# Kernel tuning notes

Measured on AMD Instinct MI355X. Metric: run time of the kernel, lower is better.

The kernel has to match this reference:

```python
import jax, jax.numpy as jnp
import numpy as np

B, C, H, W = 8, 384, 32, 32
HEADS = 12


def _relative_position_index(h, w):
    coords_h = np.arange(h)
    coords_w = np.arange(w)
    coords = np.stack(np.meshgrid(coords_h, coords_w, indexing='ij'))  # [2,h,w]
    flat = coords.reshape(2, -1)  # [2, N]
    rel = flat[:, :, None] - flat[:, None, :]  # [2, N, N]
    rel = rel.transpose(1, 2, 0)  # [N, N, 2]
    rel[:, :, 0] += h - 1
    rel[:, :, 1] += w - 1
    rel[:, :, 0] *= 2 * w - 1
    return rel.sum(-1).astype(np.int32)  # [N, N]


def setup_inputs() -> dict:
    key = jax.random.key(0)
    ks = jax.random.split(key, 6)
    std = 0.02
    x = jax.random.normal(ks[0], (B, C, H, W), dtype=jnp.float32)
    q_w = jax.random.normal(ks[1], (C, C), dtype=jnp.float32) * std
    q_b = jnp.zeros((C,), dtype=jnp.float32)
    kv_w = jax.random.normal(ks[2], (2 * C, C), dtype=jnp.float32) * std
    kv_b = jnp.zeros((2 * C,), dtype=jnp.float32)
    proj_w = jax.random.normal(ks[3], (C, C), dtype=jnp.float32) * std
    proj_b = jnp.zeros((C,), dtype=jnp.float32)
    n_table = (2 * H - 1) * (2 * W - 1)
    rpb_table = jax.random.normal(ks[4], (n_table, HEADS), dtype=jnp.float32) * std
    rel_index = jnp.asarray(_relative_position_index(H, W))  # [N, N] int32
    return {"x": x, "q_w": q_w, "q_b": q_b, "kv_w": kv_w, "kv_b": kv_b,
            "proj_w": proj_w, "proj_b": proj_b, "rpb_table": rpb_table,
            "rel_index": rel_index}


def reference(x, q_w, q_b, kv_w, kv_b, proj_w, proj_b, rpb_table, rel_index):
    b, c, h, w = x.shape
    n = h * w
    heads = rpb_table.shape[-1]
    hd = c // heads
    scale = hd ** (-0.5)

    xf = x.reshape(b, c, n)  # 1x1 conv == per-pixel matmul
    q = jnp.einsum('dc,bcn->bdn', q_w, xf) + q_b[:, None]
    q = q.reshape(b, heads, hd, n).transpose(0, 1, 3, 2)  # [b,h,n,hd]
    kv = jnp.einsum('dc,bcn->bdn', kv_w, xf) + kv_b[:, None]
    kv = kv.reshape(b, 2, heads, hd, n)
    k = kv[:, 0].transpose(0, 1, 3, 2)  # [b,h,n,hd]
    v = kv[:, 1].transpose(0, 1, 3, 2)

    attn = jnp.einsum('bhnd,bhmd->bhnm', q, k) * scale  # [b,h,n,n]
    bias = rpb_table[rel_index.reshape(-1)].reshape(n, n, heads)
    bias = bias.transpose(2, 0, 1)  # [h,n,n]
    attn = jax.nn.softmax(attn + bias[None], axis=-1)

    out = jnp.einsum('bhnm,bhmd->bhnd', attn, v)
    out = out.transpose(0, 1, 3, 2).reshape(b, c, h, w)
    out = jnp.einsum('dc,bchw->bdhw', proj_w, out) + proj_b[None, :, None, None]
    return out
```

## Files before the change

kernel.cpp:

```cpp
#include <hip/hip_runtime.h>
#include <hip/hip_bf16.h>

#define B_  8
#define C_  384
#define N_  1024
#define NH_ 12
#define HD_ 32
#define D3_ 1152

typedef __bf16 bf16x8 __attribute__((ext_vector_type(8)));
typedef float  f32x4  __attribute__((ext_vector_type(4)));

typedef const __attribute__((address_space(1))) unsigned int guint;
typedef __attribute__((address_space(3))) unsigned int luint;

__device__ __forceinline__ float b2f(ushort u) {
    return __uint_as_float(((unsigned int)u) << 16);
}
__device__ __forceinline__ ushort f2b(float f) {
    unsigned int i = __float_as_uint(f);
    unsigned int r = i + 0x7fffu + ((i >> 16) & 1u);
    return (ushort)(r >> 16);
}

#if __has_builtin(__builtin_amdgcn_exp2f)
#define EXP2 __builtin_amdgcn_exp2f
#else
#define EXP2 exp2f
#endif

__device__ __forceinline__ void gl2lds16(const void* g, void* l) {
    __builtin_amdgcn_global_load_lds((guint*)g, (luint*)l, 16, 0, 0);
}

__global__ __launch_bounds__(256) void setup(
    const float* __restrict__ x, const float* __restrict__ q_w,
    const float* __restrict__ kv_w, const float* __restrict__ proj_w,
    const float* __restrict__ q_b, const float* __restrict__ kv_b,
    const float* __restrict__ tab,
    ushort* __restrict__ xT, ushort* __restrict__ biasL,
    ushort* __restrict__ Wall, ushort* __restrict__ PW,
    float* __restrict__ ballf)
{
    __shared__ ushort T[64 * 72];
    const int bx = blockIdx.x, tid = threadIdx.x;

    if (bx < 3072) {
        const float C2 = 1.4426950408889634f;
        int gid = bx * 256 + tid;
        int lane = gid & 63;
        int mc = (gid >> 6) & 15;
        int qs = (gid >> 10) & 63;
        int h  = gid >> 16;
        int quad = lane >> 4, l16 = lane & 15;
        int q = qs * 16 + l16;
        int qy = q >> 5, qx = q & 31;
        union { uint4 u[2]; ushort us[16]; } o;
        #pragma unroll
        for (int t = 0; t < 4; ++t) {
            #pragma unroll
            for (int r = 0; r < 4; ++r) {
                int m = mc * 64 + t * 16 + quad * 4 + r;
                int my = m >> 5, mx = m & 31;
                int dy = qy - my + 31, dx = qx - mx + 31;
                float v = tab[(size_t)(dy * 63 + dx) * NH_ + h] * C2;
                o.us[t * 4 + r] = f2b(v);
            }
        }
        ushort* dst = biasL + (size_t)gid * 16;
        *(uint4*)dst = o.u[0];
        *(uint4*)(dst + 8) = o.u[1];
    } else if (bx < 3840) {
        int t = bx - 3072;
        int nx = t & 15, cy = (t >> 4) % 6, b = t / 96;
        int n0 = nx * 64, c0 = cy * 64;
        {
            int i = tid >> 2;
            int ns = (tid & 3) * 16;
            const float* src = x + ((size_t)b * C_ + c0 + i) * N_ + n0 + ns;
            #pragma unroll
            for (int k4 = 0; k4 < 4; ++k4) {
                float4 f = *(const float4*)(src + k4 * 4);
                T[(ns + k4 * 4 + 0) * 72 + i] = f2b(f.x);
                T[(ns + k4 * 4 + 1) * 72 + i] = f2b(f.y);
                T[(ns + k4 * 4 + 2) * 72 + i] = f2b(f.z);
                T[(ns + k4 * 4 + 3) * 72 + i] = f2b(f.w);
            }
        }
        __syncthreads();
        {
            int j = tid >> 2;
            int cs = (tid & 3) * 16;
            ushort* dst = xT + ((size_t)b * N_ + n0 + j) * C_ + c0 + cs;
            *(uint4*)dst       = *(const uint4*)&T[j * 72 + cs];
            *(uint4*)(dst + 8) = *(const uint4*)&T[j * 72 + cs + 8];
        }
    } else {
        const int NW4 = 110592, NP4 = 36864, NB4 = 288;
        int t = (bx - 3840) * 256 + tid;
        if (t < NW4) {
            int e = t * 4;
            float4 f = (e < 147456) ? *(const float4*)(q_w + e)
                                    : *(const float4*)(kv_w + e - 147456);
            union { uint2 u; ushort s[4]; } o;
            o.s[0] = f2b(f.x); o.s[1] = f2b(f.y); o.s[2] = f2b(f.z); o.s[3] = f2b(f.w);
            *(uint2*)(Wall + e) = o.u;
        } else if (t < NW4 + NP4) {
            int e = (t - NW4) * 4;
            float4 f = *(const float4*)(proj_w + e);
            union { uint2 u; ushort s[4]; } o;
            o.s[0] = f2b(f.x); o.s[1] = f2b(f.y); o.s[2] = f2b(f.z); o.s[3] = f2b(f.w);
            *(uint2*)(PW + e) = o.u;
        } else if (t < NW4 + NP4 + NB4) {
            int e = (t - NW4 - NP4) * 4;
            float4 f = (e < 384) ? *(const float4*)(q_b + e)
                                 : *(const float4*)(kv_b + e - 384);
            *(float4*)(ballf + e) = f;
        }
    }
}

__global__ __launch_bounds__(256) void qkv_gemm3(
    const ushort* __restrict__ xT, const ushort* __restrict__ Wall,
    const float* __restrict__ ballf, ushort* __restrict__ Qt,
    ushort* __restrict__ Kt, ushort* __restrict__ Vtmp)
{
    const int b = blockIdx.z, n0 = blockIdx.x * 128, d0 = blockIdx.y * 128;
    __shared__ ushort As[128 * 32];
    __shared__ ushort Bs[128 * 32];
    const int tid = threadIdx.x;
    const int lane = tid & 63, wave = tid >> 6;
    const int quad = lane >> 4, l16 = lane & 15;
    const int wn = (wave & 1) * 64, wd = (wave >> 1) * 64;

    f32x4 acc[4][4] = {};
    const ushort* xb = xT + ((size_t)b * N_ + n0) * C_;
    const ushort* wb = Wall + (size_t)d0 * C_;
    const int rowA = wave * 16 + (lane >> 2);
    const int fstage = ((lane >> 2) ^ (lane >> 4)) & 3;
    const int coff = ((lane & 3) ^ fstage) * 8;
    const int fread = ((l16 & 3) ^ ((l16 >> 2) & 3));

    for (int c0 = 0; c0 < C_; c0 += 32) {
        #pragma unroll
        for (int k = 0; k < 2; ++k) {
            gl2lds16(xb + (size_t)(k * 64 + rowA) * C_ + c0 + coff,
                     &As[(size_t)(k * 256 + wave * 64) * 8]);
            gl2lds16(wb + (size_t)(k * 64 + rowA) * C_ + c0 + coff,
                     &Bs[(size_t)(k * 256 + wave * 64) * 8]);
        }
        __syncthreads();
        bf16x8 af[4], bfr[4];
        #pragma unroll
        for (int i = 0; i < 4; ++i)
            af[i] = *(const bf16x8*)&As[(wn + i * 16 + l16) * 32 + (quad ^ fread) * 8];
        #pragma unroll
        for (int j = 0; j < 4; ++j)
            bfr[j] = *(const bf16x8*)&Bs[(wd + j * 16 + l16) * 32 + (quad ^ fread) * 8];
        #pragma unroll
        for (int i = 0; i < 4; ++i)
            #pragma unroll
            for (int j = 0; j < 4; ++j)
                acc[i][j] = __builtin_amdgcn_mfma_f32_16x16x32_bf16(af[i], bfr[j], acc[i][j], 0, 0, 0);
        __syncthreads();
    }

    ushort* dst; int reg0;
    if (d0 < 384)      { dst = Qt;   reg0 = 0; }
    else if (d0 < 768) { dst = Kt;   reg0 = 384; }
    else               { dst = Vtmp; reg0 = 768; }
    const int hb = (d0 - reg0) >> 5;
    #pragma unroll
    for (int j = 0; j < 4; ++j) {
        int dloc = wd + j * 16 + l16;
        int h = hb + (dloc >> 5), dc = dloc & 31;
        float bv = ballf[d0 + dloc];
        size_t base = ((size_t)(b * NH_ + h) * N_) * 32 + dc;
        #pragma unroll
        for (int i = 0; i < 4; ++i) {
            int nbase = n0 + wn + i * 16 + quad * 4;
            #pragma unroll
            for (int r = 0; r < 4; ++r)
                dst[base + (size_t)(nbase + r) * 32] = f2b(acc[i][j][r] + bv);
        }
    }
}

__global__ __launch_bounds__(256) void vtrans(
    const ushort* __restrict__ Vtmp, ushort* __restrict__ Vtc)
{
    const int mc = blockIdx.x, bh = blockIdx.y;
    __shared__ ushort T[32 * 80];
    const int tid = threadIdx.x;
    {
        int row = tid >> 2;
        int dcs = (tid & 3) * 8;
        union { uint4 u; ushort s[8]; } a;
        a.u = *(const uint4*)(Vtmp + ((size_t)bh * N_ + mc * 64 + row) * 32 + dcs);
        #pragma unroll
        for (int k = 0; k < 8; ++k) T[(dcs + k) * 80 + row] = a.s[k];
    }
    __syncthreads();
    {
        int kc = tid >> 7, dc = (tid >> 2) & 31, mm8 = (tid & 3) * 8;
        *(uint4*)(Vtc + ((size_t)(bh * 16 + mc) * 2 + kc) * 1024 + dc * 32 + mm8) =
            *(const uint4*)&T[dc * 80 + kc * 32 + mm8];
    }
}

__global__ __launch_bounds__(256) void attn3(
    const ushort* __restrict__ Qt, const ushort* __restrict__ Kt,
    const ushort* __restrict__ Vtc, const ushort* __restrict__ biasL,
    ushort* __restrict__ O)
{
    const int bid = blockIdx.x;
    const int nx = bid & 7;
    const int h  = (bid >> 3) % NH_;
    const int b  = bid / 96;
    __shared__ ushort Pa[8192];

    const int tid = threadIdx.x;
    const int lane = tid & 63, wave = tid >> 6;
    const int quad = lane >> 4, l16 = lane & 15;
    const int bh = b * NH_ + h;
    const int qs0 = nx * 8 + wave * 2;

    const ushort* Kbh = Kt + (size_t)bh * N_ * 32;
    const ushort* Vbh = Vtc + (size_t)bh * 16 * 2048;

    bf16x8 qf[2];
    #pragma unroll
    for (int st = 0; st < 2; ++st)
        qf[st] = *(const bf16x8*)(Qt + ((size_t)bh * N_ + (qs0 + st) * 16 + l16) * 32 + quad * 8);

    const ushort* bp[2];
    #pragma unroll
    for (int st = 0; st < 2; ++st)
        bp[st] = biasL + ((size_t)(h * 64 + qs0 + st) * 16 * 64 + lane) * 16;

    f32x4 oacc[2][2] = {};
    float rs[2] = {0.f, 0.f};

    ushort* PwBase = &Pa[wave * 2048];
    const int pswz = l16 & 0xE;
    const float C1 = 0.17677669529663687f * 1.4426950408889634f;
    const f32x4 zero = {0.f, 0.f, 0.f, 0.f};

    for (int mc = 0; mc < 16; ++mc) {
        const ushort* kp = Kbh + mc * 64 * 32;
        bf16x8 k0 = *(const bf16x8*)(kp + (0 * 16 + l16) * 32 + quad * 8);
        bf16x8 k1 = *(const bf16x8*)(kp + (1 * 16 + l16) * 32 + quad * 8);
        bf16x8 k2 = *(const bf16x8*)(kp + (2 * 16 + l16) * 32 + quad * 8);
        bf16x8 k3 = *(const bf16x8*)(kp + (3 * 16 + l16) * 32 + quad * 8);
        const ushort* vp = Vbh + mc * 2048;
        bf16x8 va[2][2];
        #pragma unroll
        for (int kc = 0; kc < 2; ++kc)
            #pragma unroll
            for (int dt = 0; dt < 2; ++dt)
                va[kc][dt] = *(const bf16x8*)(vp + kc * 1024 + (dt * 16 + l16) * 32 + quad * 8);
        union { uint4 u[2]; ushort us[16]; } bw[2];
        #pragma unroll
        for (int st = 0; st < 2; ++st) {
            bw[st].u[0] = *(const uint4*)(bp[st] + mc * 1024);
            bw[st].u[1] = *(const uint4*)(bp[st] + mc * 1024 + 8);
        }

        #pragma unroll
        for (int st = 0; st < 2; ++st) {
            f32x4 s0 = __builtin_amdgcn_mfma_f32_16x16x32_bf16(k0, qf[st], zero, 0, 0, 0);
            f32x4 s1 = __builtin_amdgcn_mfma_f32_16x16x32_bf16(k1, qf[st], zero, 0, 0, 0);
            f32x4 s2 = __builtin_amdgcn_mfma_f32_16x16x32_bf16(k2, qf[st], zero, 0, 0, 0);
            f32x4 s3 = __builtin_amdgcn_mfma_f32_16x16x32_bf16(k3, qf[st], zero, 0, 0, 0);

            ushort* Pw = PwBase + st * 1024;
            f32x4 sv[4] = {s0, s1, s2, s3};
            #pragma unroll
            for (int t = 0; t < 4; ++t) {
                float p0 = EXP2(sv[t][0] * C1 + b2f(bw[st].us[t * 4 + 0]));
                float p1 = EXP2(sv[t][1] * C1 + b2f(bw[st].us[t * 4 + 1]));
                float p2 = EXP2(sv[t][2] * C1 + b2f(bw[st].us[t * 4 + 2]));
                float p3 = EXP2(sv[t][3] * C1 + b2f(bw[st].us[t * 4 + 3]));
                rs[st] += (p0 + p1) + (p2 + p3);
                uint2 w;
                w.x = (unsigned)f2b(p0) | ((unsigned)f2b(p1) << 16);
                w.y = (unsigned)f2b(p2) | ((unsigned)f2b(p3) << 16);
                *(uint2*)(Pw + l16 * 64 + (((t * 4 + quad) ^ pswz) * 4)) = w;
            }
            #pragma unroll
            for (int kc = 0; kc < 2; ++kc) {
                bf16x8 pb = *(const bf16x8*)(Pw + l16 * 64 + (((kc * 8 + quad * 2) ^ pswz) * 4));
                oacc[st][0] = __builtin_amdgcn_mfma_f32_16x16x32_bf16(va[kc][0], pb, oacc[st][0], 0, 0, 0);
                oacc[st][1] = __builtin_amdgcn_mfma_f32_16x16x32_bf16(va[kc][1], pb, oacc[st][1], 0, 0, 0);
            }
        }
    }

    #pragma unroll
    for (int st = 0; st < 2; ++st) {
        float s = rs[st];
        s += __shfl_xor(s, 16, 64);
        s += __shfl_xor(s, 32, 64);
        rs[st] = 1.0f / s;
    }

    #pragma unroll
    for (int st = 0; st < 2; ++st) {
        int q = (qs0 + st) * 16 + l16;
        ushort* ob = O + ((size_t)(b * N_ + q)) * C_ + h * HD_;
        #pragma unroll
        for (int dt = 0; dt < 2; ++dt) {
            float v0 = oacc[st][dt][0] * rs[st];
            float v1 = oacc[st][dt][1] * rs[st];
            float v2 = oacc[st][dt][2] * rs[st];
            float v3 = oacc[st][dt][3] * rs[st];
            uint2 w;
            w.x = (unsigned)f2b(v0) | ((unsigned)f2b(v1) << 16);
            w.y = (unsigned)f2b(v2) | ((unsigned)f2b(v3) << 16);
            *(uint2*)(ob + dt * 16 + quad * 4) = w;
        }
    }
}

__global__ __launch_bounds__(256) void proj_gemm3(
    const ushort* __restrict__ O, const ushort* __restrict__ PW,
    const float* __restrict__ pb, float* __restrict__ out)
{
    const int b = blockIdx.z, n0 = blockIdx.x * 128, d0 = blockIdx.y * 128;
    __shared__ ushort As[128 * 32];
    __shared__ ushort Bs[128 * 32];
    const int tid = threadIdx.x;
    const int lane = tid & 63, wave = tid >> 6;
    const int quad = lane >> 4, l16 = lane & 15;
    const int wa = (wave & 1) * 64, wb = (wave >> 1) * 64;

    f32x4 acc[4][4] = {};
    const ushort* ab = PW + (size_t)d0 * C_;
    const ushort* bbp = O + ((size_t)b * N_ + n0) * C_;
    const int rowA = wave * 16 + (lane >> 2);
    const int fstage = ((lane >> 2) ^ (lane >> 4)) & 3;
    const int coff = ((lane & 3) ^ fstage) * 8;
    const int fread = ((l16 & 3) ^ ((l16 >> 2) & 3));

    for (int c0 = 0; c0 < C_; c0 += 32) {
        #pragma unroll
        for (int k = 0; k < 2; ++k) {
            gl2lds16(ab + (size_t)(k * 64 + rowA) * C_ + c0 + coff,
                     &As[(size_t)(k * 256 + wave * 64) * 8]);
            gl2lds16(bbp + (size_t)(k * 64 + rowA) * C_ + c0 + coff,
                     &Bs[(size_t)(k * 256 + wave * 64) * 8]);
        }
        __syncthreads();
        bf16x8 af[4], bfr[4];
        #pragma unroll
        for (int i = 0; i < 4; ++i)
            af[i] = *(const bf16x8*)&As[(wa + i * 16 + l16) * 32 + (quad ^ fread) * 8];
        #pragma unroll
        for (int j = 0; j < 4; ++j)
            bfr[j] = *(const bf16x8*)&Bs[(wb + j * 16 + l16) * 32 + (quad ^ fread) * 8];
        #pragma unroll
        for (int i = 0; i < 4; ++i)
            #pragma unroll
            for (int j = 0; j < 4; ++j)
                acc[i][j] = __builtin_amdgcn_mfma_f32_16x16x32_bf16(af[i], bfr[j], acc[i][j], 0, 0, 0);
        __syncthreads();
    }

    #pragma unroll
    for (int i = 0; i < 4; ++i) {
        #pragma unroll
        for (int r = 0; r < 4; ++r) {
            int d = d0 + wa + i * 16 + quad * 4 + r;
            float bv = pb[d];
            float* op = out + ((size_t)b * C_ + d) * N_ + n0 + wb;
            #pragma unroll
            for (int j = 0; j < 4; ++j)
                op[j * 16 + l16] = acc[i][j][r] + bv;
        }
    }
}

extern "C" void kernel_launch(void* const* d_in, const int* in_sizes, int n_in,
                              void* d_out, int out_size, void* d_ws, size_t ws_size,
                              hipStream_t stream)
{
    const float* x      = (const float*)d_in[0];
    const float* q_w    = (const float*)d_in[1];
    const float* q_b    = (const float*)d_in[2];
    const float* kv_w   = (const float*)d_in[3];
    const float* kv_b   = (const float*)d_in[4];
    const float* proj_w = (const float*)d_in[5];
    const float* proj_b = (const float*)d_in[6];
    const float* rpb    = (const float*)d_in[7];
    float* out = (float*)d_out;

    char* ws = (char*)d_ws;
    ushort* xT    = (ushort*)(ws);
    ushort* Qt    = (ushort*)(ws +  6291456);
    ushort* Kt    = (ushort*)(ws + 12582912);
    ushort* Vtmp  = (ushort*)(ws + 18874368);
    ushort* Vtc   = (ushort*)(ws + 25165824);
    ushort* biasL = (ushort*)(ws + 31457280);
    ushort* Wall  = (ushort*)(ws + 56623104);
    ushort* PW    = (ushort*)(ws + 57507840);
    float*  ballf = (float*) (ws + 57802752);
    ushort* O     = Vtmp;

    setup      <<<dim3(4418), 256, 0, stream>>>(x, q_w, kv_w, proj_w, q_b, kv_b, rpb,
                                                xT, biasL, Wall, PW, ballf);
    qkv_gemm3  <<<dim3(8, 9, B_), 256, 0, stream>>>(xT, Wall, ballf, Qt, Kt, Vtmp);
    vtrans     <<<dim3(16, 96), 256, 0, stream>>>(Vtmp, Vtc);
    attn3      <<<dim3(768), 256, 0, stream>>>(Qt, Kt, Vtc, biasL, O);
    proj_gemm3 <<<dim3(8, 3, B_), 256, 0, stream>>>(O, PW, proj_b, out);
}
```

Before: 168.1 us.

## Gather relative-position bias from LDS table instead of materialized bias matrix

Drops the precomputed 12x1024x1024 bf16 bias tensor (about 25MB written in setup and read back in attention). Each attention block now stages a per-head, log2e-scaled float table of 3969 entries in LDS and gathers the bias directly via index arithmetic. The bias is fed as the MFMA accumulator init, and the softmax scale is folded into Q at the QKV GEMM epilogue, which removes per-element FMAs in the exp path. Block ordering changes so that blocks sharing a head are spread differently. The cost is scattered LDS reads, which may cause bank conflicts, plus an extra 16KB of LDS per block that could reduce occupancy.

New measurement: 157.0 us. 6.6% less time.

```diff
diff --git a/kernel.cpp b/kernel.cpp
--- a/kernel.cpp
+++ b/kernel.cpp
@@ -33,45 +33,23 @@
     __builtin_amdgcn_global_load_lds((guint*)g, (luint*)l, 16, 0, 0);
 }
 
+#define C1_ 0.25505654204433796f
+#define C2_ 1.4426950408889634f
+
 __global__ __launch_bounds__(256) void setup(
     const float* __restrict__ x, const float* __restrict__ q_w,
     const float* __restrict__ kv_w, const float* __restrict__ proj_w,
     const float* __restrict__ q_b, const float* __restrict__ kv_b,
     const float* __restrict__ tab,
-    ushort* __restrict__ xT, ushort* __restrict__ biasL,
+    ushort* __restrict__ xT, float* __restrict__ tabT,
     ushort* __restrict__ Wall, ushort* __restrict__ PW,
     float* __restrict__ ballf)
 {
     __shared__ ushort T[64 * 72];
     const int bx = blockIdx.x, tid = threadIdx.x;
 
-    if (bx < 3072) {
-        const float C2 = 1.4426950408889634f;
-        int gid = bx * 256 + tid;
-        int lane = gid & 63;
-        int mc = (gid >> 6) & 15;
-        int qs = (gid >> 10) & 63;
-        int h  = gid >> 16;
-        int quad = lane >> 4, l16 = lane & 15;
-        int q = qs * 16 + l16;
-        int qy = q >> 5, qx = q & 31;
-        union { uint4 u[2]; ushort us[16]; } o;
-        #pragma unroll
-        for (int t = 0; t < 4; ++t) {
-            #pragma unroll
-            for (int r = 0; r < 4; ++r) {
-                int m = mc * 64 + t * 16 + quad * 4 + r;
-                int my = m >> 5, mx = m & 31;
-                int dy = qy - my + 31, dx = qx - mx + 31;
-                float v = tab[(size_t)(dy * 63 + dx) * NH_ + h] * C2;
-                o.us[t * 4 + r] = f2b(v);
-            }
-        }
-        ushort* dst = biasL + (size_t)gid * 16;
-        *(uint4*)dst = o.u[0];
-        *(uint4*)(dst + 8) = o.u[1];
-    } else if (bx < 3840) {
-        int t = bx - 3072;
+    if (bx < 768) {
+        int t = bx;
         int nx = t & 15, cy = (t >> 4) % 6, b = t / 96;
         int n0 = nx * 64, c0 = cy * 64;
         {
@@ -95,9 +73,9 @@
             *(uint4*)dst       = *(const uint4*)&T[j * 72 + cs];
             *(uint4*)(dst + 8) = *(const uint4*)&T[j * 72 + cs + 8];
         }
-    } else {
+    } else if (bx < 1346) {
         const int NW4 = 110592, NP4 = 36864, NB4 = 288;
-        int t = (bx - 3840) * 256 + tid;
+        int t = (bx - 768) * 256 + tid;
         if (t < NW4) {
             int e = t * 4;
             float4 f = (e < 147456) ? *(const float4*)(q_w + e)
@@ -117,6 +95,13 @@
                                  : *(const float4*)(kv_b + e - 384);
             *(float4*)(ballf + e) = f;
         }
+    } else {
+        int h = bx - 1346;
+        for (int i = tid; i < 3969; i += 256) {
+            int dyf = i / 63;
+            int src = 3906 + i - 126 * dyf;
+            tabT[h * 3969 + i] = tab[(size_t)src * NH_ + h] * C2_;
+        }
     }
 }
 
@@ -169,6 +154,7 @@
     if (d0 < 384)      { dst = Qt;   reg0 = 0; }
     else if (d0 < 768) { dst = Kt;   reg0 = 384; }
     else               { dst = Vtmp; reg0 = 768; }
+    const float sc = (d0 < 384) ? C1_ : 1.0f;
     const int hb = (d0 - reg0) >> 5;
     #pragma unroll
     for (int j = 0; j < 4; ++j) {
@@ -181,7 +167,7 @@
             int nbase = n0 + wn + i * 16 + quad * 4;
             #pragma unroll
             for (int r = 0; r < 4; ++r)
-                dst[base + (size_t)(nbase + r) * 32] = f2b(acc[i][j][r] + bv);
+                dst[base + (size_t)(nbase + r) * 32] = f2b((acc[i][j][r] + bv) * sc);
         }
     }
 }
@@ -208,43 +194,58 @@
     }
 }
 
-__global__ __launch_bounds__(256) void attn3(
+__global__ __launch_bounds__(256) void attn4(
     const ushort* __restrict__ Qt, const ushort* __restrict__ Kt,
-    const ushort* __restrict__ Vtc, const ushort* __restrict__ biasL,
+    const ushort* __restrict__ Vtc, const float* __restrict__ tabT,
     ushort* __restrict__ O)
 {
     const int bid = blockIdx.x;
-    const int nx = bid & 7;
-    const int h  = (bid >> 3) % NH_;
-    const int b  = bid / 96;
+    const int bh96 = bid % 96;
+    const int nx = bid / 96;
+    const int b = bh96 / 12, h = bh96 % 12;
+
+    __shared__ float tabL[3972];
     __shared__ ushort Pa[8192];
 
     const int tid = threadIdx.x;
     const int lane = tid & 63, wave = tid >> 6;
     const int quad = lane >> 4, l16 = lane & 15;
     const int bh = b * NH_ + h;
+
+    {
+        const float* th = tabT + h * 3969;
+        for (int i = tid; i < 3969; i += 256) tabL[i] = th[i];
+    }
+    __syncthreads();
+
     const int qs0 = nx * 8 + wave * 2;
-
     const ushort* Kbh = Kt + (size_t)bh * N_ * 32;
     const ushort* Vbh = Vtc + (size_t)bh * 16 * 2048;
 
     bf16x8 qf[2];
-    #pragma unroll
-    for (int st = 0; st < 2; ++st)
-        qf[st] = *(const bf16x8*)(Qt + ((size_t)bh * N_ + (qs0 + st) * 16 + l16) * 32 + quad * 8);
-
-    const ushort* bp[2];
-    #pragma unroll
-    for (int st = 0; st < 2; ++st)
-        bp[st] = biasL + ((size_t)(h * 64 + qs0 + st) * 16 * 64 + lane) * 16;
+    int ib[2];
+    #pragma unroll
+    for (int st = 0; st < 2; ++st) {
+        int q = (qs0 + st) * 16 + l16;
+        qf[st] = *(const bf16x8*)(Qt + ((size_t)bh * N_ + q) * 32 + quad * 8);
+        int qy = q >> 5, qx = q & 31;
+        ib[st] = (31 - qy) * 63 + qx + 31;
+    }
+
+    int off_tr[16];
+    #pragma unroll
+    for (int t = 0; t < 4; ++t)
+        #pragma unroll
+        for (int r = 0; r < 4; ++r) {
+            int ml = t * 16 + quad * 4 + r;
+            off_tr[t * 4 + r] = (ml >> 5) * 63 - (ml & 31);
+        }
 
     f32x4 oacc[2][2] = {};
     float rs[2] = {0.f, 0.f};
 
     ushort* PwBase = &Pa[wave * 2048];
     const int pswz = l16 & 0xE;
-    const float C1 = 0.17677669529663687f * 1.4426950408889634f;
-    const f32x4 zero = {0.f, 0.f, 0.f, 0.f};
 
     for (int mc = 0; mc < 16; ++mc) {
         const ushort* kp = Kbh + mc * 64 * 32;
@@ -259,28 +260,31 @@
             #pragma unroll
             for (int dt = 0; dt < 2; ++dt)
                 va[kc][dt] = *(const bf16x8*)(vp + kc * 1024 + (dt * 16 + l16) * 32 + quad * 8);
-        union { uint4 u[2]; ushort us[16]; } bw[2];
+
         #pragma unroll
         for (int st = 0; st < 2; ++st) {
-            bw[st].u[0] = *(const uint4*)(bp[st] + mc * 1024);
-            bw[st].u[1] = *(const uint4*)(bp[st] + mc * 1024 + 8);
-        }
-
-        #pragma unroll
-        for (int st = 0; st < 2; ++st) {
-            f32x4 s0 = __builtin_amdgcn_mfma_f32_16x16x32_bf16(k0, qf[st], zero, 0, 0, 0);
-            f32x4 s1 = __builtin_amdgcn_mfma_f32_16x16x32_bf16(k1, qf[st], zero, 0, 0, 0);
-            f32x4 s2 = __builtin_amdgcn_mfma_f32_16x16x32_bf16(k2, qf[st], zero, 0, 0, 0);
-            f32x4 s3 = __builtin_amdgcn_mfma_f32_16x16x32_bf16(k3, qf[st], zero, 0, 0, 0);
+            const int ibm = ib[st] + mc * 126;
+            f32x4 cb[4];
+            #pragma unroll
+            for (int t = 0; t < 4; ++t) {
+                cb[t][0] = tabL[ibm + off_tr[t * 4 + 0]];
+                cb[t][1] = tabL[ibm + off_tr[t * 4 + 1]];
+                cb[t][2] = tabL[ibm + off_tr[t * 4 + 2]];
+                cb[t][3] = tabL[ibm + off_tr[t * 4 + 3]];
+            }
+            f32x4 s0 = __builtin_amdgcn_mfma_f32_16x16x32_bf16(k0, qf[st], cb[0], 0, 0, 0);
+            f32x4 s1 = __builtin_amdgcn_mfma_f32_16x16x32_bf16(k1, qf[st], cb[1], 0, 0, 0);
+            f32x4 s2 = __builtin_amdgcn_mfma_f32_16x16x32_bf16(k2, qf[st], cb[2], 0, 0, 0);
+            f32x4 s3 = __builtin_amdgcn_mfma_f32_16x16x32_bf16(k3, qf[st], cb[3], 0, 0, 0);
 
             ushort* Pw = PwBase + st * 1024;
             f32x4 sv[4] = {s0, s1, s2, s3};
             #pragma unroll
             for (int t = 0; t < 4; ++t) {
-                float p0 = EXP2(sv[t][0] * C1 + b2f(bw[st].us[t * 4 + 0]));
-                float p1 = EXP2(sv[t][1] * C1 + b2f(bw[st].us[t * 4 + 1]));
-                float p2 = EXP2(sv[t][2] * C1 + b2f(bw[st].us[t * 4 + 2]));
-                float p3 = EXP2(sv[t][3] * C1 + b2f(bw[st].us[t * 4 + 3]));
+                float p0 = EXP2(sv[t][0]);
+                float p1 = EXP2(sv[t][1]);
+                float p2 = EXP2(sv[t][2]);
+                float p3 = EXP2(sv[t][3]);
                 rs[st] += (p0 + p1) + (p2 + p3);
                 uint2 w;
                 w.x = (unsigned)f2b(p0) | ((unsigned)f2b(p1) << 16);
@@ -400,16 +404,16 @@
     ushort* Kt    = (ushort*)(ws + 12582912);
     ushort* Vtmp  = (ushort*)(ws + 18874368);
     ushort* Vtc   = (ushort*)(ws + 25165824);
-    ushort* biasL = (ushort*)(ws + 31457280);
-    ushort* Wall  = (ushort*)(ws + 56623104);
-    ushort* PW    = (ushort*)(ws + 57507840);
-    float*  ballf = (float*) (ws + 57802752);
+    float*  tabT  = (float*) (ws + 31457280);
+    ushort* Wall  = (ushort*)(ws + 31647808);
+    ushort* PW    = (ushort*)(ws + 32532544);
+    float*  ballf = (float*) (ws + 32827456);
     ushort* O     = Vtmp;
 
-    setup      <<<dim3(4418), 256, 0, stream>>>(x, q_w, kv_w, proj_w, q_b, kv_b, rpb,
-                                                xT, biasL, Wall, PW, ballf);
+    setup      <<<dim3(1358), 256, 0, stream>>>(x, q_w, kv_w, proj_w, q_b, kv_b, rpb,
+                                                xT, tabT, Wall, PW, ballf);
     qkv_gemm3  <<<dim3(8, 9, B_), 256, 0, stream>>>(xT, Wall, ballf, Qt, Kt, Vtmp);
     vtrans     <<<dim3(16, 96), 256, 0, stream>>>(Vtmp, Vtc);
-    attn3      <<<dim3(768), 256, 0, stream>>>(Qt, Kt, Vtc, biasL, O);
+    attn4      <<<dim3(768), 256, 0, stream>>>(Qt, Kt, Vtc, tabT, O);
     proj_gemm3 <<<dim3(8, 3, B_), 256, 0, stream>>>(O, PW, proj_b, out);
 }
```
